# Performance work log

Measured on AMD Instinct MI355X. Metric: run time of the kernel, lower is better.

## Reference

```python
import jax, jax.numpy as jnp
import numpy as np

MODEL_DIM = 1024
N_HEADS = 16
HEAD_DIM = 64  # q_dim == k_dim == v_dim


def setup_inputs() -> dict:
    key = jax.random.key(0)
    ks = jax.random.split(key, 7)
    B, S = 4, 2048
    scale = 1.0 / np.sqrt(MODEL_DIM)
    return {
        "q": jax.random.normal(ks[0], (B, S, MODEL_DIM), dtype=jnp.float32),
        "k": jax.random.normal(ks[1], (B, S, MODEL_DIM), dtype=jnp.float32),
        "v": jax.random.normal(ks[2], (B, S, MODEL_DIM), dtype=jnp.float32),
        # Linear weights stored as [out, in] like torch; no biases.
        "wq": jax.random.normal(ks[3], (N_HEADS * HEAD_DIM, MODEL_DIM), dtype=jnp.float32) * scale,
        "wk": jax.random.normal(ks[4], (N_HEADS * HEAD_DIM, MODEL_DIM), dtype=jnp.float32) * scale,
        "wv": jax.random.normal(ks[5], (N_HEADS * HEAD_DIM, MODEL_DIM), dtype=jnp.float32) * scale,
        "wo": jax.random.normal(ks[6], (MODEL_DIM, N_HEADS * HEAD_DIM), dtype=jnp.float32) * scale,
    }


def reference(q, k, v, wq, wk, wv, wo):
    B, Sq, _ = q.shape
    Sk = k.shape[1]
    # projections: [B,S,D] @ W^T -> [B,S,H*dh] -> [B,H,S,dh]
    qh = (q @ wq.T).reshape(B, Sq, N_HEADS, HEAD_DIM).transpose(0, 2, 1, 3)
    kh = (k @ wk.T).reshape(B, Sk, N_HEADS, HEAD_DIM).transpose(0, 2, 1, 3)
    vh = (v @ wv.T).reshape(B, Sk, N_HEADS, HEAD_DIM).transpose(0, 2, 1, 3)
    # scores [B,H,Sq,Sk], scaled by sqrt(k_dim)
    scores = jnp.einsum('bhqd,bhkd->bhqk', qh, kh) / jnp.sqrt(jnp.float32(HEAD_DIM))
    attn = jax.nn.softmax(scores, axis=-1)
    ctx = jnp.einsum('bhqk,bhkd->bhqd', attn, vh)  # [B,H,Sq,dh]
    ctx = ctx.transpose(0, 2, 1, 3).reshape(B, Sq, N_HEADS * HEAD_DIM)
    return ctx @ wo.T
```

## Files before the change

kernel.cpp:

```cpp
#include <hip/hip_runtime.h>
#include <cstdint>
#include <cstddef>


typedef _Float16 f16x8 __attribute__((ext_vector_type(8)));
typedef _Float16 f16x4 __attribute__((ext_vector_type(4)));
typedef _Float16 f16x2 __attribute__((ext_vector_type(2)));
typedef __fp16 h16x2 __attribute__((ext_vector_type(2)));
typedef float f32x4 __attribute__((ext_vector_type(4)));
typedef float f32x16 __attribute__((ext_vector_type(16)));
typedef unsigned u32x4 __attribute__((ext_vector_type(4)));
typedef int i32x2 __attribute__((ext_vector_type(2)));

#define LDS_CAST(p) ((__attribute__((address_space(3))) void*)(p))
#define GLB_CAST(p) ((const __attribute__((address_space(1))) void*)(p))

__device__ __forceinline__ void gload_lds16(const void* g, void* l) {
  __builtin_amdgcn_global_load_lds(GLB_CAST(g), LDS_CAST(l), 16, 0, 0);
}

__device__ __forceinline__ float fexp2(float x) {
#if __has_builtin(__builtin_amdgcn_exp2f)
  return __builtin_amdgcn_exp2f(x);
#else
  return exp2f(x);
#endif
}

__device__ __forceinline__ f16x2 pkrtz(float a, float b) {
  h16x2 r = __builtin_amdgcn_cvt_pkrtz(a, b);
  return __builtin_bit_cast(f16x2, r);
}

__device__ __forceinline__ float dot2acc(f16x2 a, float acc) {
#if __has_builtin(__builtin_amdgcn_fdot2)
  const f16x2 one2 = {(_Float16)1.0f, (_Float16)1.0f};
  return __builtin_amdgcn_fdot2(a, one2, acc, false);
#else
  return acc + (float)a[0] + (float)a[1];
#endif
}

__device__ __forceinline__ void pl32swap(unsigned& a, unsigned& b) {
#if __has_builtin(__builtin_amdgcn_permlane32_swap)
  i32x2 r = __builtin_amdgcn_permlane32_swap((int)a, (int)b, false, false);
  a = (unsigned)r[0];
  b = (unsigned)r[1];
#else
  asm("v_permlane32_swap_b32 %0, %1" : "+v"(a), "+v"(b));
#endif
}

__global__ void cvt_all(const float* __restrict__ q, const float* __restrict__ k,
                        const float* __restrict__ v, const float* __restrict__ wq,
                        const float* __restrict__ wk, const float* __restrict__ wv,
                        const float* __restrict__ wo, _Float16* __restrict__ oq,
                        _Float16* __restrict__ ok, _Float16* __restrict__ ov,
                        _Float16* __restrict__ owq, _Float16* __restrict__ owk,
                        _Float16* __restrict__ owv, _Float16* __restrict__ owo) {
  int id = blockIdx.x;
  const float* in;
  _Float16* out;
  int base;
  if (id < 24576) {
    int z = id >> 13;
    base = (id & 8191) * 256;
    in = z == 0 ? q : z == 1 ? k : v;
    out = z == 0 ? oq : z == 1 ? ok : ov;
  } else {
    int id2 = id - 24576;
    int z = id2 >> 10;
    base = (id2 & 1023) * 256;
    in = z == 0 ? wq : z == 1 ? wk : z == 2 ? wv : wo;
    out = z == 0 ? owq : z == 1 ? owk : z == 2 ? owv : owo;
  }
  int i = base + threadIdx.x;
  float4 vv = ((const float4*)in)[i];
  f16x4 o = {(_Float16)vv.x, (_Float16)vv.y, (_Float16)vv.z, (_Float16)vv.w};
  ((f16x4*)out)[i] = o;
}

template <int MODE>
__device__ __forceinline__ void gemm_core(const _Float16* __restrict__ A,
                                          const _Float16* __restrict__ W,
                                          void* __restrict__ C, float scale,
                                          _Float16* As, _Float16* Bs) {
  constexpr int K = 1024, N = 1024;
  const int tid = threadIdx.x;
  const int wid = tid >> 6;
  const int lane = tid & 63;
  const int quad = lane >> 4;
  const int l16 = lane & 15;
  const int wm = wid >> 1;
  const int wn = wid & 1;

  int lin = blockIdx.y * 8 + blockIdx.x;
  int swz = (lin & 7) * 64 + (lin >> 3);
  const int m0 = (swz >> 3) * 128;
  const int n0 = (swz & 7) * 128;

  const _Float16* Ag = A + (size_t)m0 * K;
  const _Float16* Bg = W + (size_t)n0 * K;

  f32x4 acc[4][4];
#pragma unroll
  for (int i = 0; i < 4; i++)
#pragma unroll
    for (int j = 0; j < 4; j++) acc[i][j] = (f32x4){0.f, 0.f, 0.f, 0.f};

  const int lrow = lane >> 2;
  const int swsrc = ((lane & 3) ^ ((lane >> 3) & 3)) * 8;

  auto stage = [&](int buf, int k0) {
#pragma unroll
    for (int i = 0; i < 2; i++) {
      int issue = wid * 2 + i;
      gload_lds16(Ag + (size_t)(issue * 16 + lrow) * K + k0 + swsrc,
                  &As[buf * 4096 + issue * 512]);
      gload_lds16(Bg + (size_t)(issue * 16 + lrow) * K + k0 + swsrc,
                  &Bs[buf * 4096 + issue * 512]);
    }
  };

  stage(0, 0);
  stage(1, 32);

  const int swq = (quad ^ ((l16 >> 1) & 3)) * 8;
  int rb = 0;

  for (int t = 0; t < 32; t++) {
    if (t < 31)
      asm volatile("s_waitcnt vmcnt(4)" ::: "memory");
    else
      asm volatile("s_waitcnt vmcnt(0)" ::: "memory");
    __builtin_amdgcn_s_barrier();
    asm volatile("" ::: "memory");

    if (t < 30) {
      int sb = rb + 2;
      if (sb >= 3) sb -= 3;
      stage(sb, (t + 2) * 32);
    }

    const _Float16* Ab = &As[rb * 4096];
    const _Float16* Bb = &Bs[rb * 4096];
    f16x8 af[4], bfr[4];
#pragma unroll
    for (int mt = 0; mt < 4; mt++)
      af[mt] = *(const f16x8*)&Ab[(wm * 64 + mt * 16 + l16) * 32 + swq];
#pragma unroll
    for (int nt = 0; nt < 4; nt++)
      bfr[nt] = *(const f16x8*)&Bb[(wn * 64 + nt * 16 + l16) * 32 + swq];
#pragma unroll
    for (int mt = 0; mt < 4; mt++)
#pragma unroll
      for (int nt = 0; nt < 4; nt++)
        acc[mt][nt] = __builtin_amdgcn_mfma_f32_16x16x32_f16(
            af[mt], bfr[nt], acc[mt][nt], 0, 0, 0);

    rb = (rb == 2) ? 0 : rb + 1;
  }

#pragma unroll
  for (int mt = 0; mt < 4; mt++) {
#pragma unroll
    for (int nt = 0; nt < 4; nt++) {
#pragma unroll
      for (int r = 0; r < 4; r++) {
        int m = m0 + wm * 64 + mt * 16 + quad * 4 + r;
        int n = n0 + wn * 64 + nt * 16 + l16;
        float v = acc[mt][nt][r] * scale;
        if (MODE == 0) {
          ((float*)C)[(size_t)m * N + n] = v;
        } else {
          int b = m >> 11, s = m & 2047;
          int h = n >> 6, dd = n & 63;
          size_t bh = (size_t)(b * 16 + h);
          if (MODE == 1) {
            ((_Float16*)C)[(bh * 2048 + s) * 64 + dd] = (_Float16)v;
          } else if (MODE == 3) {
            int kt2 = s >> 5, l32k = s & 31;
            int s4 = dd >> 4, hi8 = (dd >> 3) & 1, j = dd & 7;
            size_t idx = (bh * 32 + (kt2 >> 1)) * 8192 +
                         (((kt2 & 1) * 4 + s4) * 512) + (hi8 * 32 + l32k) * 8 +
                         j;
            ((_Float16*)C)[idx] = (_Float16)v;
          } else {
            int kt = s >> 6, ks = (s >> 4) & 3, hi8 = (s >> 3) & 1, j = s & 7;
            int dt = dd >> 5, l32v = dd & 31;
            size_t idx = (bh * 32 + kt) * 8192 + 4096 + ((dt * 4 + ks) * 512) +
                         (hi8 * 32 + l32v) * 8 + j;
            ((_Float16*)C)[idx] = (_Float16)v;
          }
        }
      }
    }
  }
}

__global__ __launch_bounds__(256) void gemm_qkv(
    const _Float16* __restrict__ qb, const _Float16* __restrict__ kb,
    const _Float16* __restrict__ vb, const _Float16* __restrict__ wq,
    const _Float16* __restrict__ wk, const _Float16* __restrict__ wv,
    _Float16* __restrict__ Qh, _Float16* __restrict__ KVf) {
  __shared__ _Float16 As[3 * 128 * 32];
  __shared__ _Float16 Bs[3 * 128 * 32];
  if (blockIdx.z == 0)
    gemm_core<1>(qb, wq, Qh, 0.18033688f, As, Bs);
  else if (blockIdx.z == 1)
    gemm_core<3>(kb, wk, KVf, 1.0f, As, Bs);
  else
    gemm_core<4>(vb, wv, KVf, 1.0f, As, Bs);
}

__global__ __launch_bounds__(256) void gemm_wo(const _Float16* __restrict__ ctx,
                                               const _Float16* __restrict__ wo,
                                               float* __restrict__ out) {
  __shared__ _Float16 As[3 * 128 * 32];
  __shared__ _Float16 Bs[3 * 128 * 32];
  gemm_core<0>(ctx, wo, out, 1.0f, As, Bs);
}

__global__ __launch_bounds__(256, 3) void attn_kernel(
    const _Float16* __restrict__ Qh, const _Float16* __restrict__ KVf,
    _Float16* __restrict__ ctx) {
  __shared__ _Float16 sKV[3][8192];

  const int qt = blockIdx.x;
  const int bh = blockIdx.y;
  const int tid = threadIdx.x;
  const int wid = tid >> 6;
  const int lane = tid & 63;
  const int l32 = lane & 31;
  const int hi = lane >> 5;

  const _Float16* Qg = Qh + ((size_t)bh * 2048 + qt * 128 + wid * 32) * 64;
  const _Float16* KVb = KVf + (size_t)bh * 262144;

  f16x8 aq[4];
#pragma unroll
  for (int s = 0; s < 4; s++)
    aq[s] = *(const f16x8*)(Qg + (size_t)l32 * 64 + s * 16 + hi * 8);

  f32x16 acc[2];
#pragma unroll
  for (int i = 0; i < 16; i++) {
    acc[0][i] = 0.f;
    acc[1][i] = 0.f;
  }
  float lsA = 0.f, lsB = 0.f;

  auto stage = [&](int buf, int kt) {
    const _Float16* t = KVb + (size_t)kt * 8192;
#pragma unroll
    for (int i = 0; i < 4; i++) {
      int c = wid * 4 + i;
      gload_lds16(t + c * 512 + lane * 8, &sKV[buf][c * 512]);
    }
  };

  stage(0, 0);
  int cur = 0;

  for (int kt = 0; kt < 32; kt++) {
    int nxt = (cur == 2) ? 0 : cur + 1;
    if (kt < 31) {
      stage(nxt, kt + 1);
      asm volatile("s_waitcnt vmcnt(4)" ::: "memory");
    } else {
      asm volatile("s_waitcnt vmcnt(0)" ::: "memory");
    }
    __builtin_amdgcn_s_barrier();
    asm volatile("" ::: "memory");

    const _Float16* Ks = sKV[cur];
    const _Float16* Vs = sKV[cur] + 4096;

    f16x8 kf0[4], kf1[4];
#pragma unroll
    for (int s = 0; s < 4; s++) {
      kf0[s] = *(const f16x8*)&Ks[(0 * 4 + s) * 512 + lane * 8];
      kf1[s] = *(const f16x8*)&Ks[(4 + s) * 512 + lane * 8];
    }

    f32x16 s0, s1;
#pragma unroll
    for (int i = 0; i < 16; i++) {
      s0[i] = 0.f;
      s1[i] = 0.f;
    }
#pragma unroll
    for (int s = 0; s < 4; s++) {
      s0 = __builtin_amdgcn_mfma_f32_32x32x16_f16(kf0[s], aq[s], s0, 0, 0, 0);
      s1 = __builtin_amdgcn_mfma_f32_32x32x16_f16(kf1[s], aq[s], s1, 0, 0, 0);
    }

    f16x8 vf0[4], vf1[4];
#pragma unroll
    for (int g = 0; g < 4; g++) {
      vf0[g] = *(const f16x8*)&Vs[(0 * 4 + g) * 512 + lane * 8];
      vf1[g] = *(const f16x8*)&Vs[(4 + g) * 512 + lane * 8];
    }

    unsigned hw[2][8];
#pragma unroll
    for (int i = 0; i < 8; i++) {
      f16x2 hh = pkrtz(fexp2(s0[2 * i]), fexp2(s0[2 * i + 1]));
      if (i & 1)
        lsB = dot2acc(hh, lsB);
      else
        lsA = dot2acc(hh, lsA);
      hw[0][i] = __builtin_bit_cast(unsigned, hh);
    }
#pragma unroll
    for (int i = 0; i < 8; i++) {
      f16x2 hh = pkrtz(fexp2(s1[2 * i]), fexp2(s1[2 * i + 1]));
      if (i & 1)
        lsB = dot2acc(hh, lsB);
      else
        lsA = dot2acc(hh, lsA);
      hw[1][i] = __builtin_bit_cast(unsigned, hh);
    }

#pragma unroll
    for (int st = 0; st < 2; st++)
#pragma unroll
      for (int kh = 0; kh < 2; kh++) {
        unsigned w0 = hw[st][4 * kh + 0], w2 = hw[st][4 * kh + 2];
        unsigned w1 = hw[st][4 * kh + 1], w3 = hw[st][4 * kh + 3];
        pl32swap(w0, w2);
        pl32swap(w1, w3);
        u32x4 wv4 = {w0, w1, w2, w3};
        f16x8 pfrag = __builtin_bit_cast(f16x8, wv4);
        int g = st * 2 + kh;
        acc[0] = __builtin_amdgcn_mfma_f32_32x32x16_f16(vf0[g], pfrag, acc[0],
                                                        0, 0, 0);
        acc[1] = __builtin_amdgcn_mfma_f32_32x32x16_f16(vf1[g], pfrag, acc[1],
                                                        0, 0, 0);
      }

    cur = nxt;
  }

  float lsum = lsA + lsB;
  float l = lsum + __shfl_xor(lsum, 32);
  float inv = 1.f / l;
  const int b = bh >> 4, h = bh & 15;
  int q = qt * 128 + wid * 32 + l32;
  _Float16* outp = ctx + ((size_t)b * 2048 + q) * 1024 + h * 64;
#pragma unroll
  for (int dt = 0; dt < 2; dt++)
#pragma unroll
    for (int g = 0; g < 4; g++) {
      f16x4 o;
#pragma unroll
      for (int c = 0; c < 4; c++) o[c] = (_Float16)(acc[dt][g * 4 + c] * inv);
      *(f16x4*)(outp + dt * 32 + g * 8 + hi * 4) = o;
    }
}

extern "C" void kernel_launch(void* const* d_in, const int* in_sizes, int n_in,
                              void* d_out, int out_size, void* d_ws,
                              size_t ws_size, hipStream_t stream) {
  const float* q = (const float*)d_in[0];
  const float* k = (const float*)d_in[1];
  const float* v = (const float*)d_in[2];
  const float* wq = (const float*)d_in[3];
  const float* wk = (const float*)d_in[4];
  const float* wv = (const float*)d_in[5];
  const float* wo = (const float*)d_in[6];
  float* out = (float*)d_out;

  const size_t SD = (size_t)8192 * 1024;
  const size_t WSZ = (size_t)1024 * 1024;

  _Float16* ws = (_Float16*)d_ws;
  _Float16* qb = ws;
  _Float16* kb = ws + 1 * SD;
  _Float16* vb = ws + 2 * SD;
  _Float16* Qh = ws + 3 * SD;
  _Float16* KVf = ws + 4 * SD;
  _Float16* ctx = ws + 6 * SD;
  _Float16* wqb = ws + 7 * SD;
  _Float16* wkb = wqb + WSZ;
  _Float16* wvb = wqb + 2 * WSZ;
  _Float16* wob = wqb + 3 * WSZ;

  cvt_all<<<dim3(28672), 256, 0, stream>>>(q, k, v, wq, wk, wv, wo, qb, kb, vb,
                                           wqb, wkb, wvb, wob);

  gemm_qkv<<<dim3(8, 64, 3), 256, 0, stream>>>(qb, kb, vb, wqb, wkb, wvb, Qh,
                                               KVf);

  attn_kernel<<<dim3(16, 64), 256, 0, stream>>>(Qh, KVf, ctx);

  gemm_wo<<<dim3(8, 64), 256, 0, stream>>>(ctx, wob, out);
}
```

Baseline: 342.9 us.

## Switch GEMM pipeline from triple to double buffering with unrolled ping-pong

Replaces the three-stage rotating LDS pipeline in the shared GEMM core with a two-buffer ping-pong loop, unrolled by two so buffer addresses are compile-time constants. Each step issues the next tile load before computing on the current buffer, then waits for all loads and barriers. LDS use drops to two stages and launch bounds request four blocks per CU, aiming for higher occupancy. The cost is a shallower prefetch: a full vmcnt(0) wait every step exposes more global load latency.

```diff
diff --git a/kernel.cpp b/kernel.cpp
--- a/kernel.cpp
+++ b/kernel.cpp
@@ -111,39 +111,20 @@
   const int lrow = lane >> 2;
   const int swsrc = ((lane & 3) ^ ((lane >> 3) & 3)) * 8;
 
-  auto stage = [&](int buf, int k0) {
+  auto stage = [&](_Float16* Ad, _Float16* Bd, int k0) {
 #pragma unroll
     for (int i = 0; i < 2; i++) {
       int issue = wid * 2 + i;
       gload_lds16(Ag + (size_t)(issue * 16 + lrow) * K + k0 + swsrc,
-                  &As[buf * 4096 + issue * 512]);
+                  Ad + issue * 512);
       gload_lds16(Bg + (size_t)(issue * 16 + lrow) * K + k0 + swsrc,
-                  &Bs[buf * 4096 + issue * 512]);
+                  Bd + issue * 512);
     }
   };
 
-  stage(0, 0);
-  stage(1, 32);
-
   const int swq = (quad ^ ((l16 >> 1) & 3)) * 8;
-  int rb = 0;
-
-  for (int t = 0; t < 32; t++) {
-    if (t < 31)
-      asm volatile("s_waitcnt vmcnt(4)" ::: "memory");
-    else
-      asm volatile("s_waitcnt vmcnt(0)" ::: "memory");
-    __builtin_amdgcn_s_barrier();
-    asm volatile("" ::: "memory");
-
-    if (t < 30) {
-      int sb = rb + 2;
-      if (sb >= 3) sb -= 3;
-      stage(sb, (t + 2) * 32);
-    }
-
-    const _Float16* Ab = &As[rb * 4096];
-    const _Float16* Bb = &Bs[rb * 4096];
+
+  auto compute = [&](const _Float16* Ab, const _Float16* Bb) {
     f16x8 af[4], bfr[4];
 #pragma unroll
     for (int mt = 0; mt < 4; mt++)
@@ -157,9 +138,33 @@
       for (int nt = 0; nt < 4; nt++)
         acc[mt][nt] = __builtin_amdgcn_mfma_f32_16x16x32_f16(
             af[mt], bfr[nt], acc[mt][nt], 0, 0, 0);
-
-    rb = (rb == 2) ? 0 : rb + 1;
+  };
+
+  _Float16* A0 = As;
+  _Float16* A1 = As + 4096;
+  _Float16* B0 = Bs;
+  _Float16* B1 = Bs + 4096;
+
+  stage(A0, B0, 0);
+  asm volatile("s_waitcnt vmcnt(0)" ::: "memory");
+  __builtin_amdgcn_s_barrier();
+
+  for (int g = 0; g < 15; g++) {
+    int t2 = g * 2;
+    stage(A1, B1, (t2 + 1) * 32);
+    compute(A0, B0);
+    asm volatile("s_waitcnt vmcnt(0)" ::: "memory");
+    __builtin_amdgcn_s_barrier();
+    stage(A0, B0, (t2 + 2) * 32);
+    compute(A1, B1);
+    asm volatile("s_waitcnt vmcnt(0)" ::: "memory");
+    __builtin_amdgcn_s_barrier();
   }
+  stage(A1, B1, 31 * 32);
+  compute(A0, B0);
+  asm volatile("s_waitcnt vmcnt(0)" ::: "memory");
+  __builtin_amdgcn_s_barrier();
+  compute(A1, B1);
 
 #pragma unroll
   for (int mt = 0; mt < 4; mt++) {
@@ -198,13 +203,13 @@
   }
 }
 
-__global__ __launch_bounds__(256) void gemm_qkv(
+__global__ __launch_bounds__(256, 4) void gemm_qkv(
     const _Float16* __restrict__ qb, const _Float16* __restrict__ kb,
     const _Float16* __restrict__ vb, const _Float16* __restrict__ wq,
     const _Float16* __restrict__ wk, const _Float16* __restrict__ wv,
     _Float16* __restrict__ Qh, _Float16* __restrict__ KVf) {
-  __shared__ _Float16 As[3 * 128 * 32];
-  __shared__ _Float16 Bs[3 * 128 * 32];
+  __shared__ _Float16 As[2 * 128 * 32];
+  __shared__ _Float16 Bs[2 * 128 * 32];
   if (blockIdx.z == 0)
     gemm_core<1>(qb, wq, Qh, 0.18033688f, As, Bs);
   else if (blockIdx.z == 1)
@@ -213,11 +218,11 @@
     gemm_core<4>(vb, wv, KVf, 1.0f, As, Bs);
 }
 
-__global__ __launch_bounds__(256) void gemm_wo(const _Float16* __restrict__ ctx,
-                                               const _Float16* __restrict__ wo,
-                                               float* __restrict__ out) {
-  __shared__ _Float16 As[3 * 128 * 32];
-  __shared__ _Float16 Bs[3 * 128 * 32];
+__global__ __launch_bounds__(256, 4) void gemm_wo(
+    const _Float16* __restrict__ ctx, const _Float16* __restrict__ wo,
+    float* __restrict__ out) {
+  __shared__ _Float16 As[2 * 128 * 32];
+  __shared__ _Float16 Bs[2 * 128 * 32];
   gemm_core<0>(ctx, wo, out, 1.0f, As, Bs);
 }
 
```

After: 333.8 us. -2.7%, faster.
